# Kernel tuning notes

Hardware: AMD Instinct MI355X
Metric: run time of the kernel (lower is better)

## Reference

```python
import jax, jax.numpy as jnp
import numpy as np

B, L, D, H = 4, 1024, 1024, 16
DK = D // H  # per-head dim = d_q = d_k = d_v = 64


def setup_inputs() -> dict:
    key = jax.random.key(0)
    ks = jax.random.split(key, 11)
    s = 0.02
    return {
        "query": jax.random.normal(ks[0], (B, L, D), jnp.float32),
        "key_in": jax.random.normal(ks[1], (B, L, D), jnp.float32),
        "value": jax.random.normal(ks[2], (B, L, D), jnp.float32),
        # per-head Q/K projection weights stacked: [H, D, DK]
        "wq": jax.random.normal(ks[3], (H, D, DK), jnp.float32) * s,
        "bq": jax.random.normal(ks[4], (H, DK), jnp.float32) * s,
        "wk": jax.random.normal(ks[5], (H, D, DK), jnp.float32) * s,
        "bk": jax.random.normal(ks[6], (H, DK), jnp.float32) * s,
        # shared value projection: [D, DK]
        "wv": jax.random.normal(ks[7], (D, DK), jnp.float32) * s,
        "bv": jax.random.normal(ks[8], (DK,), jnp.float32) * s,
        # output projection: [DK, D]
        "wo": jax.random.normal(ks[9], (DK, D), jnp.float32) * s,
        "bo": jax.random.normal(ks[10], (D,), jnp.float32) * s,
    }


def reference(query, key_in, value, wq, bq, wk, bk, wv, bv, wo, bo):
    dk = wq.shape[-1]
    scale = 1.0 / np.sqrt(dk).astype(np.float32)
    # shared V projection: [B, L, DK]
    v_proj = value @ wv + bv
    # batched per-head Q/K projections (replaces the per-head Linear loop)
    q = jnp.einsum("bld,hdk->bhlk", query, wq) + bq[None, :, None, :]
    k = jnp.einsum("bld,hdk->bhlk", key_in, wk) + bk[None, :, None, :]
    # softmax(QK^T / sqrt(dk)) directly -- equivalent to SDPA with v=eye(L)
    scores = jnp.einsum("bhqk,bhmk->bhqm", q, k) * scale  # [B, H, Lq, Lk]
    attn = jax.nn.softmax(scores, axis=-1)
    # head_i = attn_i @ v_proj : [B, H, Lq, DK]
    heads = jnp.einsum("bhqm,bmv->bhqv", attn, v_proj)
    head_mean = heads.mean(axis=1)  # mean over heads -> [B, Lq, DK]
    output = head_mean @ wo + bo  # [B, Lq, D]
    # match torch stack(dim=2): attn -> [B, Lq, H, Lk]
    attn_out = jnp.transpose(attn, (0, 2, 1, 3))
    return output, attn_out
```

## Files before the change

### kernel.cpp

```cpp
#include <hip/hip_runtime.h>
#include <math.h>

#define NB 4
#define NL 1024
#define ND 1024
#define NH 16
#define NDK 64

typedef __attribute__((ext_vector_type(8))) short short8;
typedef __attribute__((ext_vector_type(4))) float f32x4;

__device__ inline ushort f2bf(float f) {
    uint x = __float_as_uint(f);
    x += 0x7FFFu + ((x >> 16) & 1u);
    return (ushort)(x >> 16);
}
__device__ inline float bf2f(ushort u) { return __uint_as_float(((uint)u) << 16); }

__device__ inline void gload16(const void* g, void* l) {
    __builtin_amdgcn_global_load_lds(
        (const __attribute__((address_space(1))) void*)g,
        (__attribute__((address_space(3))) void*)l, 16, 0, 0);
}

__global__ __launch_bounds__(256) void prep_kernel(
    const float* __restrict__ q, const float* __restrict__ k,
    const float* __restrict__ v,
    const float* __restrict__ wq, const float* __restrict__ wk,
    const float* __restrict__ wv,
    ushort* __restrict__ abf,
    ushort* __restrict__ wqT, ushort* __restrict__ wkT, ushort* __restrict__ wvT)
{
    __shared__ ushort tl[64][72];
    const int t = threadIdx.x;
    const int bid = blockIdx.x;

    if (bid < 6144) {
        int y = bid >> 11, x = bid & 2047;
        const float* src = (y == 0) ? q : (y == 1) ? k : v;
        size_t base = ((size_t)x * 256 + t) * 8;
        float4 a = *(const float4*)(src + base);
        float4 b = *(const float4*)(src + base + 4);
        short8 o;
        o[0] = (short)f2bf(a.x); o[1] = (short)f2bf(a.y);
        o[2] = (short)f2bf(a.z); o[3] = (short)f2bf(a.w);
        o[4] = (short)f2bf(b.x); o[5] = (short)f2bf(b.y);
        o[6] = (short)f2bf(b.z); o[7] = (short)f2bf(b.w);
        *(short8*)(abf + (size_t)y * (NB * NL * ND) + base) = o;
        return;
    }

    int id = bid - 6144;
    int d0 = (id & 15) * 64;
    int y = id >> 4;
    const float* src; ushort* dst; int h;
    if (y < 16)      { src = wq + (size_t)y * ND * NDK;        dst = wqT; h = y; }
    else if (y < 32) { src = wk + (size_t)(y - 16) * ND * NDK; dst = wkT; h = y - 16; }
    else             { src = wv;                               dst = wvT; h = 0; }

    int r = t >> 2, c0 = (t & 3) * 16;
    const float* s = src + (size_t)(d0 + r) * NDK + c0;
    #pragma unroll
    for (int j = 0; j < 16; j += 4) {
        float4 vv4 = *(const float4*)(s + j);
        tl[c0 + j + 0][r] = f2bf(vv4.x);
        tl[c0 + j + 1][r] = f2bf(vv4.y);
        tl[c0 + j + 2][r] = f2bf(vv4.z);
        tl[c0 + j + 3][r] = f2bf(vv4.w);
    }
    __syncthreads();
    int vv = t >> 2, lc = (t & 3) * 16;
    ushort* d = dst + ((size_t)h * 64 + vv) * ND + d0 + lc;
    #pragma unroll
    for (int j = 0; j < 16; j += 8) {
        short8 o;
        #pragma unroll
        for (int e = 0; e < 8; ++e) o[e] = (short)tl[vv][lc + j + e];
        *(short8*)(d + j) = o;
    }
    if (y == 32) {
        ushort* zp = wvT + ((size_t)(64 + (t >> 2))) * ND + d0 + (t & 3) * 16;
        short8 z8 = {0,0,0,0,0,0,0,0};
        *(short8*)(zp) = z8;
        *(short8*)(zp + 8) = z8;
    }
}

__global__ __launch_bounds__(256) void proj_gemm(
    const ushort* __restrict__ abf,
    const ushort* __restrict__ wqT, const ushort* __restrict__ wkT,
    const ushort* __restrict__ wvT,
    const float* __restrict__ bq, const float* __restrict__ bk,
    const float* __restrict__ bv,
    ushort* __restrict__ q_all, ushort* __restrict__ k_all,
    ushort* __restrict__ vT)
{
    __shared__ char lds[49152];

    int id = blockIdx.x;
    int wg = (id & 7) * 136 + (id >> 3);
    int z, mt, nt;
    if (wg < 512)       { z = 0; mt = wg >> 3; nt = wg & 7; }
    else if (wg < 1024) { z = 1; int r2 = wg - 512; mt = r2 >> 3; nt = r2 & 7; }
    else                { z = 2; mt = wg - 1024; nt = 0; }

    const ushort* A; const ushort* Bw; const float* bias; float scale;
    if (z == 0)      { A = abf;                    Bw = wqT; bias = bq; scale = 0.125f; }
    else if (z == 1) { A = abf + NB * NL * ND;     Bw = wkT; bias = bk; scale = 1.0f; }
    else             { A = abf + 2 * NB * NL * ND; Bw = wvT; bias = bv; scale = 1.0f; }
    ushort* C = (z == 0) ? q_all : k_all;

    const int t = threadIdx.x;
    const int w = t >> 6, l = t & 63;
    const int lo16 = l & 15, hi = l >> 4;
    const int wm = w >> 1, wn = w & 1;
    const int m0 = mt * 64, n0 = nt * 128;

    f32x4 acc[2][4];
    #pragma unroll
    for (int mi = 0; mi < 2; ++mi)
        #pragma unroll
        for (int ni = 0; ni < 4; ++ni) acc[mi][ni] = (f32x4){0.f, 0.f, 0.f, 0.f};

    const int lrow = l >> 3;
    const uint lcol = ((uint)(l & 7) * 16u) ^ (((uint)lrow) << 4);

    #pragma unroll
    for (int i = 0; i < 2; ++i) {
        int s = w * 2 + i;
        gload16(A + (size_t)(m0 + s * 8 + lrow) * ND + (lcol >> 1), lds + s * 1024);
    }
    #pragma unroll
    for (int i = 0; i < 4; ++i) {
        int s = w * 4 + i;
        gload16(Bw + (size_t)(n0 + s * 8 + lrow) * ND + (lcol >> 1), lds + 8192 + s * 1024);
    }
    __syncthreads();

    int cur = 0;
    for (int kt = 0; kt < 16; ++kt) {
        if (kt < 15) {
            const int k1 = (kt + 1) * 64;
            const int nb = (cur ^ 1) * 24576;
            #pragma unroll
            for (int i = 0; i < 2; ++i) {
                int s = w * 2 + i;
                gload16(A + (size_t)(m0 + s * 8 + lrow) * ND + k1 + (lcol >> 1), lds + nb + s * 1024);
            }
            #pragma unroll
            for (int i = 0; i < 4; ++i) {
                int s = w * 4 + i;
                gload16(Bw + (size_t)(n0 + s * 8 + lrow) * ND + k1 + (lcol >> 1), lds + nb + 8192 + s * 1024);
            }
        }
        const int cb = cur * 24576;
        #pragma unroll
        for (int ks = 0; ks < 2; ++ks) {
            short8 Af[2], Bf[4];
            #pragma unroll
            for (int mi = 0; mi < 2; ++mi) {
                int row = wm * 32 + mi * 16 + lo16;
                uint off = ((uint)row * 128u + (uint)(ks * 64 + hi * 16)) ^ (((uint)(row & 7)) << 4);
                Af[mi] = *(short8*)(lds + cb + off);
            }
            #pragma unroll
            for (int ni = 0; ni < 4; ++ni) {
                int row = wn * 64 + ni * 16 + lo16;
                uint off = ((uint)row * 128u + (uint)(ks * 64 + hi * 16)) ^ (((uint)(row & 7)) << 4);
                Bf[ni] = *(short8*)(lds + cb + 8192 + off);
            }
            __builtin_amdgcn_s_setprio(1);
            #pragma unroll
            for (int mi = 0; mi < 2; ++mi)
                #pragma unroll
                for (int ni = 0; ni < 4; ++ni)
                    acc[mi][ni] = __builtin_amdgcn_mfma_f32_16x16x32_bf16(
                        Af[mi], Bf[ni], acc[mi][ni], 0, 0, 0);
            __builtin_amdgcn_s_setprio(0);
        }
        __syncthreads();
        cur ^= 1;
    }

    if (z == 2) {
        if (wn == 0) {
            #pragma unroll
            for (int ni = 0; ni < 4; ++ni) {
                int n = ni * 16 + lo16;
                float bs = bias[n];
                #pragma unroll
                for (int mi = 0; mi < 2; ++mi) {
                    int mbase = m0 + wm * 32 + mi * 16 + hi * 4;
                    int b = mbase >> 10, ll = mbase & 1023;
                    uint u0 = (uint)f2bf(acc[mi][ni][0] + bs) | ((uint)f2bf(acc[mi][ni][1] + bs) << 16);
                    uint u1 = (uint)f2bf(acc[mi][ni][2] + bs) | ((uint)f2bf(acc[mi][ni][3] + bs) << 16);
                    *(uint2*)(vT + ((size_t)b * NDK + n) * NL + ll) = make_uint2(u0, u1);
                }
            }
        }
        return;
    }

    ushort* cst = (ushort*)lds;
    const int n0w = wn * 64;
    #pragma unroll
    for (int ni = 0; ni < 4; ++ni) {
        int nl = n0w + ni * 16 + lo16;
        float bs = bias[n0 + nl];
        #pragma unroll
        for (int mi = 0; mi < 2; ++mi) {
            int mlb = wm * 32 + mi * 16 + hi * 4;
            #pragma unroll
            for (int r = 0; r < 4; ++r)
                cst[(mlb + r) * 128 + nl] = f2bf((acc[mi][ni][r] + bs) * scale);
        }
    }
    __syncthreads();
    #pragma unroll
    for (int i = 0; i < 4; ++i) {
        int unit = t + 256 * i;
        int row = unit >> 4, s8 = unit & 15;
        short8 v = *(short8*)(cst + row * 128 + s8 * 8);
        int m = m0 + row, n = n0 + s8 * 8;
        int b = m >> 10, ll = m & 1023, h = n >> 6, dk = n & 63;
        *(short8*)(C + (((size_t)b * NH + h) * NL + ll) * NDK + dk) = v;
    }
}

__global__ __launch_bounds__(256) void attn_mfma_kernel(
    const ushort* __restrict__ q_all, const ushort* __restrict__ k_all,
    const ushort* __restrict__ vT,
    float* __restrict__ attn, ushort* __restrict__ heads)
{
    __shared__ char raw[65536 + 640];
    float* smv  = (float*)(raw + 65536);
    float* invb = (float*)(raw + 65536 + 512);

    const int t = threadIdx.x;
    const int kh = t >> 6, l = t & 63;
    const int hi = l >> 4, lo = l & 15;
    const int h  = blockIdx.x;
    const int q0 = blockIdx.y * 32;
    const int b  = blockIdx.z;
    const size_t bh = ((size_t)b * NH + h) * NL;

    const int qrA = lo;
    const int qrB = 16 + lo;
    const uint swz = ((uint)(lo & 7)) << 4;

    short8 QA0 = *(const short8*)(q_all + (bh + q0 + qrA) * NDK + hi * 8);
    short8 QA1 = *(const short8*)(q_all + (bh + q0 + qrA) * NDK + 32 + hi * 8);
    short8 QB0 = *(const short8*)(q_all + (bh + q0 + qrB) * NDK + hi * 8);
    short8 QB1 = *(const short8*)(q_all + (bh + q0 + qrB) * NDK + 32 + hi * 8);

    float ssumA = 0.f, ssumB = 0.f;
    for (int kt = 0; kt < 16; ++kt) {
        const int kbase = kh * 256 + kt * 16;
        short8 Ka0 = *(const short8*)(k_all + (bh + kbase + lo) * NDK + hi * 8);
        short8 Ka1 = *(const short8*)(k_all + (bh + kbase + lo) * NDK + 32 + hi * 8);
        f32x4 sA = {0.f, 0.f, 0.f, 0.f};
        f32x4 sB = {0.f, 0.f, 0.f, 0.f};
        __builtin_amdgcn_s_setprio(1);
        sA = __builtin_amdgcn_mfma_f32_16x16x32_bf16(Ka0, QA0, sA, 0, 0, 0);
        sA = __builtin_amdgcn_mfma_f32_16x16x32_bf16(Ka1, QA1, sA, 0, 0, 0);
        sB = __builtin_amdgcn_mfma_f32_16x16x32_bf16(Ka0, QB0, sB, 0, 0, 0);
        sB = __builtin_amdgcn_mfma_f32_16x16x32_bf16(Ka1, QB1, sB, 0, 0, 0);
        __builtin_amdgcn_s_setprio(0);
        float a0 = __expf(sA[0]), a1 = __expf(sA[1]);
        float a2 = __expf(sA[2]), a3 = __expf(sA[3]);
        float b0 = __expf(sB[0]), b1 = __expf(sB[1]);
        float b2 = __expf(sB[2]), b3 = __expf(sB[3]);
        ssumA += (a0 + a1) + (a2 + a3);
        ssumB += (b0 + b1) + (b2 + b3);
        uint colb = (((uint)(kbase + hi * 4)) * 2u) ^ swz;
        *(uint2*)(raw + (uint)qrA * 2048u + colb) =
            make_uint2((uint)f2bf(a0) | ((uint)f2bf(a1) << 16),
                       (uint)f2bf(a2) | ((uint)f2bf(a3) << 16));
        *(uint2*)(raw + (uint)qrB * 2048u + colb) =
            make_uint2((uint)f2bf(b0) | ((uint)f2bf(b1) << 16),
                       (uint)f2bf(b2) | ((uint)f2bf(b3) << 16));
    }
    ssumA += __shfl_xor(ssumA, 16);
    ssumA += __shfl_xor(ssumA, 32);
    ssumB += __shfl_xor(ssumB, 16);
    ssumB += __shfl_xor(ssumB, 32);
    if (l < 16) {
        smv[kh * 32 + l]      = ssumA;
        smv[kh * 32 + 16 + l] = ssumB;
    }
    __syncthreads();
    if (t < 32) invb[t] = 1.0f / (smv[t] + smv[32 + t] + smv[64 + t] + smv[96 + t]);
    __syncthreads();

    f32x4 accA0 = {0.f,0.f,0.f,0.f}, accA1 = {0.f,0.f,0.f,0.f};
    f32x4 accA2 = {0.f,0.f,0.f,0.f}, accA3 = {0.f,0.f,0.f,0.f};
    f32x4 accB0 = {0.f,0.f,0.f,0.f}, accB1 = {0.f,0.f,0.f,0.f};
    f32x4 accB2 = {0.f,0.f,0.f,0.f}, accB3 = {0.f,0.f,0.f,0.f};
    for (int kc = 0; kc < 8; ++kc) {
        const int kchunk = kh * 256 + kc * 32;
        uint colb = (((uint)(kchunk + hi * 8)) * 2u) ^ swz;
        short8 paA = *(short8*)(raw + (uint)qrA * 2048u + colb);
        short8 paB = *(short8*)(raw + (uint)qrB * 2048u + colb);
        short8 b0 = *(const short8*)(vT + ((size_t)(b * NDK +  0 + lo)) * NL + kchunk + hi * 8);
        short8 b1 = *(const short8*)(vT + ((size_t)(b * NDK + 16 + lo)) * NL + kchunk + hi * 8);
        short8 b2 = *(const short8*)(vT + ((size_t)(b * NDK + 32 + lo)) * NL + kchunk + hi * 8);
        short8 b3 = *(const short8*)(vT + ((size_t)(b * NDK + 48 + lo)) * NL + kchunk + hi * 8);
        __builtin_amdgcn_s_setprio(1);
        accA0 = __builtin_amdgcn_mfma_f32_16x16x32_bf16(paA, b0, accA0, 0, 0, 0);
        accA1 = __builtin_amdgcn_mfma_f32_16x16x32_bf16(paA, b1, accA1, 0, 0, 0);
        accA2 = __builtin_amdgcn_mfma_f32_16x16x32_bf16(paA, b2, accA2, 0, 0, 0);
        accA3 = __builtin_amdgcn_mfma_f32_16x16x32_bf16(paA, b3, accA3, 0, 0, 0);
        accB0 = __builtin_amdgcn_mfma_f32_16x16x32_bf16(paB, b0, accB0, 0, 0, 0);
        accB1 = __builtin_amdgcn_mfma_f32_16x16x32_bf16(paB, b1, accB1, 0, 0, 0);
        accB2 = __builtin_amdgcn_mfma_f32_16x16x32_bf16(paB, b2, accB2, 0, 0, 0);
        accB3 = __builtin_amdgcn_mfma_f32_16x16x32_bf16(paB, b3, accB3, 0, 0, 0);
        __builtin_amdgcn_s_setprio(0);
        #pragma unroll
        for (int rj = 0; rj < 4; ++rj) {
            int rr = kc * 4 + rj;
            uint byteoff = (uint)rr * 2048u + (((uint)t * 8u) ^ (((uint)(rr & 7)) << 4));
            uint2 v = *(uint2*)(raw + byteoff);
            float inv = invb[rr];
            f32x4 o;
            o[0] = bf2f((ushort)(v.x & 0xFFFF)) * inv;
            o[1] = bf2f((ushort)(v.x >> 16)) * inv;
            o[2] = bf2f((ushort)(v.y & 0xFFFF)) * inv;
            o[3] = bf2f((ushort)(v.y >> 16)) * inv;
            __builtin_nontemporal_store(o,
                (f32x4*)(attn + (((size_t)b * NL + q0 + rr) * NH + h) * NL + (size_t)t * 4));
        }
    }
    __syncthreads();
    float* pvp = (float*)raw;
    #pragma unroll
    for (int r = 0; r < 4; ++r) {
        int rowA = kh * 32 + hi * 4 + r;
        pvp[rowA * 68 +  0 + lo] = accA0[r];
        pvp[rowA * 68 + 16 + lo] = accA1[r];
        pvp[rowA * 68 + 32 + lo] = accA2[r];
        pvp[rowA * 68 + 48 + lo] = accA3[r];
        int rowB = rowA + 16;
        pvp[rowB * 68 +  0 + lo] = accB0[r];
        pvp[rowB * 68 + 16 + lo] = accB1[r];
        pvp[rowB * 68 + 32 + lo] = accB2[r];
        pvp[rowB * 68 + 48 + lo] = accB3[r];
    }
    __syncthreads();
    #pragma unroll
    for (int i = 0; i < 8; ++i) {
        int idx = t + 256 * i;
        int qq = idx >> 6, vv = idx & 63;
        float s4 = pvp[qq * 68 + vv] + pvp[(32 + qq) * 68 + vv]
                 + pvp[(64 + qq) * 68 + vv] + pvp[(96 + qq) * 68 + vv];
        heads[(bh + q0 + qq) * NDK + vv] = f2bf(s4 * invb[qq]);
    }
}

__global__ __launch_bounds__(256) void out_proj_kernel(
    const ushort* __restrict__ heads, const float* __restrict__ wo,
    const float* __restrict__ bo, float* __restrict__ out)
{
    const int t = threadIdx.x;
    const int row0 = blockIdx.x * 8;
    const int b = row0 >> 10, l0 = row0 & 1023;
    __shared__ float hm[8][64];
    if (t < 128) {
        int r = t >> 4;
        int f4 = t & 15;
        float sx = 0.f, sy = 0.f, sz = 0.f, sw = 0.f;
        #pragma unroll
        for (int h = 0; h < 16; ++h) {
            uint2 v = *(const uint2*)&heads[(((size_t)b * NH + h) * NL + l0 + r) * NDK + f4 * 4];
            sx += bf2f((ushort)(v.x & 0xFFFF));
            sy += bf2f((ushort)(v.x >> 16));
            sz += bf2f((ushort)(v.y & 0xFFFF));
            sw += bf2f((ushort)(v.y >> 16));
        }
        float4 o; o.x = sx * 0.0625f; o.y = sy * 0.0625f; o.z = sz * 0.0625f; o.w = sw * 0.0625f;
        *(float4*)&hm[r][f4 * 4] = o;
    }
    __syncthreads();

    float acc[8][4];
    #pragma unroll
    for (int r = 0; r < 8; ++r)
        #pragma unroll
        for (int j = 0; j < 4; ++j) acc[r][j] = 0.f;

    for (int k = 0; k < 64; ++k) {
        float w0 = wo[(size_t)k * ND + t];
        float w1 = wo[(size_t)k * ND + t + 256];
        float w2 = wo[(size_t)k * ND + t + 512];
        float w3 = wo[(size_t)k * ND + t + 768];
        #pragma unroll
        for (int r = 0; r < 8; ++r) {
            float hv = hm[r][k];
            acc[r][0] += hv * w0;
            acc[r][1] += hv * w1;
            acc[r][2] += hv * w2;
            acc[r][3] += hv * w3;
        }
    }
    #pragma unroll
    for (int r = 0; r < 8; ++r) {
        out[((size_t)row0 + r) * ND + t      ] = acc[r][0] + bo[t];
        out[((size_t)row0 + r) * ND + t + 256] = acc[r][1] + bo[t + 256];
        out[((size_t)row0 + r) * ND + t + 512] = acc[r][2] + bo[t + 512];
        out[((size_t)row0 + r) * ND + t + 768] = acc[r][3] + bo[t + 768];
    }
}

extern "C" void kernel_launch(void* const* d_in, const int* in_sizes, int n_in,
                              void* d_out, int out_size, void* d_ws, size_t ws_size,
                              hipStream_t stream) {
    const float* query  = (const float*)d_in[0];
    const float* key_in = (const float*)d_in[1];
    const float* value  = (const float*)d_in[2];
    const float* wq     = (const float*)d_in[3];
    const float* bq     = (const float*)d_in[4];
    const float* wk     = (const float*)d_in[5];
    const float* bk     = (const float*)d_in[6];
    const float* wv     = (const float*)d_in[7];
    const float* bv     = (const float*)d_in[8];
    const float* wo     = (const float*)d_in[9];
    const float* bo     = (const float*)d_in[10];

    float* out  = (float*)d_out;
    float* attn = out + (size_t)NB * NL * ND;

    ushort* wqT    = (ushort*)d_ws;
    ushort* wkT    = wqT + (size_t)ND * NH * NDK;
    ushort* wvT    = wkT + (size_t)ND * NH * NDK;
    ushort* q_all  = wvT + (size_t)128 * ND;
    ushort* k_all  = q_all + (size_t)NB * NH * NL * NDK;
    ushort* vT     = k_all + (size_t)NB * NH * NL * NDK;
    ushort* abf    = vT + (size_t)NB * NDK * NL;
    ushort* heads  = abf;

    prep_kernel<<<dim3(6672), 256, 0, stream>>>(
        query, key_in, value, wq, wk, wv, abf, wqT, wkT, wvT);
    proj_gemm<<<dim3(1088), 256, 0, stream>>>(
        abf, wqT, wkT, wvT, bq, bk, bv, q_all, k_all, vT);
    attn_mfma_kernel<<<dim3(NH, NL / 32, NB), 256, 0, stream>>>(
        q_all, k_all, vT, attn, heads);
    out_proj_kernel<<<dim3(NB * NL / 8), 256, 0, stream>>>(
        heads, wo, bo, out);
}
```

Before: 138.6 us.

## Fuse fp32-to-bf16 activation conversion into projection GEMM A-tile loads

Drops the separate pass that converted query/key/value to bf16 in a workspace buffer. The projection GEMM now reads fp32 activations directly into registers for the next K-tile, converts them to bf16 after the current tile's MFMAs, and writes them into the swizzled LDS buffer. This removes a full write and re-read of the bf16 activation copy and shrinks the prep launch to weights only. In exchange, the GEMM reads twice the bytes per A tile through registers instead of async global-to-LDS loads, and does extra conversion work inside the main loop. Each A tile is also re-read by the eight N-tiles of its row.

Result: slower. 148.3 us (+7.0%).

```diff
diff --git a/kernel.cpp b/kernel.cpp
--- a/kernel.cpp
+++ b/kernel.cpp
@@ -24,33 +24,13 @@
 }
 
 __global__ __launch_bounds__(256) void prep_kernel(
-    const float* __restrict__ q, const float* __restrict__ k,
-    const float* __restrict__ v,
     const float* __restrict__ wq, const float* __restrict__ wk,
     const float* __restrict__ wv,
-    ushort* __restrict__ abf,
     ushort* __restrict__ wqT, ushort* __restrict__ wkT, ushort* __restrict__ wvT)
 {
     __shared__ ushort tl[64][72];
     const int t = threadIdx.x;
-    const int bid = blockIdx.x;
-
-    if (bid < 6144) {
-        int y = bid >> 11, x = bid & 2047;
-        const float* src = (y == 0) ? q : (y == 1) ? k : v;
-        size_t base = ((size_t)x * 256 + t) * 8;
-        float4 a = *(const float4*)(src + base);
-        float4 b = *(const float4*)(src + base + 4);
-        short8 o;
-        o[0] = (short)f2bf(a.x); o[1] = (short)f2bf(a.y);
-        o[2] = (short)f2bf(a.z); o[3] = (short)f2bf(a.w);
-        o[4] = (short)f2bf(b.x); o[5] = (short)f2bf(b.y);
-        o[6] = (short)f2bf(b.z); o[7] = (short)f2bf(b.w);
-        *(short8*)(abf + (size_t)y * (NB * NL * ND) + base) = o;
-        return;
-    }
-
-    int id = bid - 6144;
+    int id = blockIdx.x;
     int d0 = (id & 15) * 64;
     int y = id >> 4;
     const float* src; ushort* dst; int h;
@@ -87,7 +67,8 @@
 }
 
 __global__ __launch_bounds__(256) void proj_gemm(
-    const ushort* __restrict__ abf,
+    const float* __restrict__ query, const float* __restrict__ key_in,
+    const float* __restrict__ value,
     const ushort* __restrict__ wqT, const ushort* __restrict__ wkT,
     const ushort* __restrict__ wvT,
     const float* __restrict__ bq, const float* __restrict__ bk,
@@ -104,10 +85,10 @@
     else if (wg < 1024) { z = 1; int r2 = wg - 512; mt = r2 >> 3; nt = r2 & 7; }
     else                { z = 2; mt = wg - 1024; nt = 0; }
 
-    const ushort* A; const ushort* Bw; const float* bias; float scale;
-    if (z == 0)      { A = abf;                    Bw = wqT; bias = bq; scale = 0.125f; }
-    else if (z == 1) { A = abf + NB * NL * ND;     Bw = wkT; bias = bk; scale = 1.0f; }
-    else             { A = abf + 2 * NB * NL * ND; Bw = wvT; bias = bv; scale = 1.0f; }
+    const float* A; const ushort* Bw; const float* bias; float scale;
+    if (z == 0)      { A = query;  Bw = wqT; bias = bq; scale = 0.125f; }
+    else if (z == 1) { A = key_in; Bw = wkT; bias = bk; scale = 1.0f; }
+    else             { A = value;  Bw = wvT; bias = bv; scale = 1.0f; }
     ushort* C = (z == 0) ? q_all : k_all;
 
     const int t = threadIdx.x;
@@ -125,28 +106,43 @@
     const int lrow = l >> 3;
     const uint lcol = ((uint)(l & 7) * 16u) ^ (((uint)lrow) << 4);
 
-    #pragma unroll
-    for (int i = 0; i < 2; ++i) {
-        int s = w * 2 + i;
-        gload16(A + (size_t)(m0 + s * 8 + lrow) * ND + (lcol >> 1), lds + s * 1024);
-    }
-    #pragma unroll
-    for (int i = 0; i < 4; ++i) {
-        int s = w * 4 + i;
-        gload16(Bw + (size_t)(n0 + s * 8 + lrow) * ND + (lcol >> 1), lds + 8192 + s * 1024);
+    const int ar0 = (2 * t) >> 3, ac0 = (2 * t) & 7;
+    const int ar1 = (2 * t + 1) >> 3, ac1 = (2 * t + 1) & 7;
+    const uint aoff0 = ((uint)ar0 * 128u + (uint)ac0 * 16u) ^ (((uint)(ar0 & 7)) << 4);
+    const uint aoff1 = ((uint)ar1 * 128u + (uint)ac1 * 16u) ^ (((uint)(ar1 & 7)) << 4);
+    const float* arow0 = A + (size_t)(m0 + ar0) * ND + ac0 * 8;
+    const float* arow1 = A + (size_t)(m0 + ar1) * ND + ac1 * 8;
+
+    {
+        float4 a00 = *(const float4*)(arow0);
+        float4 a01 = *(const float4*)(arow0 + 4);
+        float4 a10 = *(const float4*)(arow1);
+        float4 a11 = *(const float4*)(arow1 + 4);
+        short8 o0, o1;
+        o0[0]=(short)f2bf(a00.x); o0[1]=(short)f2bf(a00.y); o0[2]=(short)f2bf(a00.z); o0[3]=(short)f2bf(a00.w);
+        o0[4]=(short)f2bf(a01.x); o0[5]=(short)f2bf(a01.y); o0[6]=(short)f2bf(a01.z); o0[7]=(short)f2bf(a01.w);
+        o1[0]=(short)f2bf(a10.x); o1[1]=(short)f2bf(a10.y); o1[2]=(short)f2bf(a10.z); o1[3]=(short)f2bf(a10.w);
+        o1[4]=(short)f2bf(a11.x); o1[5]=(short)f2bf(a11.y); o1[6]=(short)f2bf(a11.z); o1[7]=(short)f2bf(a11.w);
+        *(short8*)(lds + aoff0) = o0;
+        *(short8*)(lds + aoff1) = o1;
+        #pragma unroll
+        for (int i = 0; i < 4; ++i) {
+            int s = w * 4 + i;
+            gload16(Bw + (size_t)(n0 + s * 8 + lrow) * ND + (lcol >> 1), lds + 8192 + s * 1024);
+        }
     }
     __syncthreads();
 
     int cur = 0;
     for (int kt = 0; kt < 16; ++kt) {
+        float4 a00, a01, a10, a11;
+        const int nb = (cur ^ 1) * 24576;
         if (kt < 15) {
             const int k1 = (kt + 1) * 64;
-            const int nb = (cur ^ 1) * 24576;
-            #pragma unroll
-            for (int i = 0; i < 2; ++i) {
-                int s = w * 2 + i;
-                gload16(A + (size_t)(m0 + s * 8 + lrow) * ND + k1 + (lcol >> 1), lds + nb + s * 1024);
-            }
+            a00 = *(const float4*)(arow0 + k1);
+            a01 = *(const float4*)(arow0 + k1 + 4);
+            a10 = *(const float4*)(arow1 + k1);
+            a11 = *(const float4*)(arow1 + k1 + 4);
             #pragma unroll
             for (int i = 0; i < 4; ++i) {
                 int s = w * 4 + i;
@@ -177,6 +173,15 @@
                     acc[mi][ni] = __builtin_amdgcn_mfma_f32_16x16x32_bf16(
                         Af[mi], Bf[ni], acc[mi][ni], 0, 0, 0);
             __builtin_amdgcn_s_setprio(0);
+        }
+        if (kt < 15) {
+            short8 o0, o1;
+            o0[0]=(short)f2bf(a00.x); o0[1]=(short)f2bf(a00.y); o0[2]=(short)f2bf(a00.z); o0[3]=(short)f2bf(a00.w);
+            o0[4]=(short)f2bf(a01.x); o0[5]=(short)f2bf(a01.y); o0[6]=(short)f2bf(a01.z); o0[7]=(short)f2bf(a01.w);
+            o1[0]=(short)f2bf(a10.x); o1[1]=(short)f2bf(a10.y); o1[2]=(short)f2bf(a10.z); o1[3]=(short)f2bf(a10.w);
+            o1[4]=(short)f2bf(a11.x); o1[5]=(short)f2bf(a11.y); o1[6]=(short)f2bf(a11.z); o1[7]=(short)f2bf(a11.w);
+            *(short8*)(lds + nb + aoff0) = o0;
+            *(short8*)(lds + nb + aoff1) = o1;
         }
         __syncthreads();
         cur ^= 1;
@@ -434,13 +439,11 @@
     ushort* q_all  = wvT + (size_t)128 * ND;
     ushort* k_all  = q_all + (size_t)NB * NH * NL * NDK;
     ushort* vT     = k_all + (size_t)NB * NH * NL * NDK;
-    ushort* abf    = vT + (size_t)NB * NDK * NL;
-    ushort* heads  = abf;
-
-    prep_kernel<<<dim3(6672), 256, 0, stream>>>(
-        query, key_in, value, wq, wk, wv, abf, wqT, wkT, wvT);
+    ushort* heads  = vT + (size_t)NB * NDK * NL;
+
+    prep_kernel<<<dim3(528), 256, 0, stream>>>(wq, wk, wv, wqT, wkT, wvT);
     proj_gemm<<<dim3(1088), 256, 0, stream>>>(
-        abf, wqT, wkT, wvT, bq, bk, bv, q_all, k_all, vT);
+        query, key_in, value, wqT, wkT, wvT, bq, bk, bv, q_all, k_all, vT);
     attn_mfma_kernel<<<dim3(NH, NL / 32, NB), 256, 0, stream>>>(
         q_all, k_all, vT, attn, heads);
     out_proj_kernel<<<dim3(NB * NL / 8), 256, 0, stream>>>(
```

## Use bf16 MFMA for output projection with pre-transposed bf16 Wo

Applied to the files above, without the earlier changes.

The prep kernel gains 16 extra blocks that convert Wo to bf16 and transpose it to an [N][K] layout. The output projection now stages the bf16 head mean in swizzled LDS and computes each 32x256 tile with 16x16x32 bf16 MFMA instructions, replacing the scalar FP32 FMA loop over 8-row tiles. This moves the output GEMM onto matrix cores and cuts Wo read traffic. The cost is extra rounding of the head mean and Wo to bf16, plus more prep work.

Measured after the change: 136.5 us (median of 2 runs). Within noise of the previous version (-1.5%).

```diff
diff --git a/kernel.cpp b/kernel.cpp
--- a/kernel.cpp
+++ b/kernel.cpp
@@ -27,9 +27,10 @@
     const float* __restrict__ q, const float* __restrict__ k,
     const float* __restrict__ v,
     const float* __restrict__ wq, const float* __restrict__ wk,
-    const float* __restrict__ wv,
+    const float* __restrict__ wv, const float* __restrict__ wo,
     ushort* __restrict__ abf,
-    ushort* __restrict__ wqT, ushort* __restrict__ wkT, ushort* __restrict__ wvT)
+    ushort* __restrict__ wqT, ushort* __restrict__ wkT,
+    ushort* __restrict__ wvT, ushort* __restrict__ woT)
 {
     __shared__ ushort tl[64][72];
     const int t = threadIdx.x;
@@ -53,6 +54,31 @@
     int id = bid - 6144;
     int d0 = (id & 15) * 64;
     int y = id >> 4;
+
+    if (y == 33) {
+        int kr = t >> 2, c0 = (t & 3) * 16;
+        const float* s = wo + (size_t)kr * ND + d0 + c0;
+        #pragma unroll
+        for (int j = 0; j < 16; j += 4) {
+            float4 vv4 = *(const float4*)(s + j);
+            tl[c0 + j + 0][kr] = f2bf(vv4.x);
+            tl[c0 + j + 1][kr] = f2bf(vv4.y);
+            tl[c0 + j + 2][kr] = f2bf(vv4.z);
+            tl[c0 + j + 3][kr] = f2bf(vv4.w);
+        }
+        __syncthreads();
+        int vv = t >> 2, lc = (t & 3) * 16;
+        ushort* d = woT + (size_t)(d0 + vv) * NDK + lc;
+        #pragma unroll
+        for (int j = 0; j < 16; j += 8) {
+            short8 o;
+            #pragma unroll
+            for (int e = 0; e < 8; ++e) o[e] = (short)tl[vv][lc + j + e];
+            *(short8*)(d + j) = o;
+        }
+        return;
+    }
+
     const float* src; ushort* dst; int h;
     if (y < 16)      { src = wq + (size_t)y * ND * NDK;        dst = wqT; h = y; }
     else if (y < 32) { src = wk + (size_t)(y - 16) * ND * NDK; dst = wkT; h = y - 16; }
@@ -357,56 +383,66 @@
 }
 
 __global__ __launch_bounds__(256) void out_proj_kernel(
-    const ushort* __restrict__ heads, const float* __restrict__ wo,
+    const ushort* __restrict__ heads, const ushort* __restrict__ woT,
     const float* __restrict__ bo, float* __restrict__ out)
 {
+    __shared__ char lds[4096];
     const int t = threadIdx.x;
-    const int row0 = blockIdx.x * 8;
-    const int b = row0 >> 10, l0 = row0 & 1023;
-    __shared__ float hm[8][64];
-    if (t < 128) {
-        int r = t >> 4;
-        int f4 = t & 15;
-        float sx = 0.f, sy = 0.f, sz = 0.f, sw = 0.f;
+    const int w = t >> 6, l = t & 63;
+    const int lo16 = l & 15, hi = l >> 4;
+    const int rt = blockIdx.x >> 2, ct = blockIdx.x & 3;
+    const int m0 = rt * 32, n0 = ct * 256;
+    const int b = m0 >> 10, l0 = m0 & 1023;
+
+    {
+        int r = t >> 3, qd = t & 7;
+        float s[8] = {0.f,0.f,0.f,0.f,0.f,0.f,0.f,0.f};
         #pragma unroll
         for (int h = 0; h < 16; ++h) {
-            uint2 v = *(const uint2*)&heads[(((size_t)b * NH + h) * NL + l0 + r) * NDK + f4 * 4];
-            sx += bf2f((ushort)(v.x & 0xFFFF));
-            sy += bf2f((ushort)(v.x >> 16));
-            sz += bf2f((ushort)(v.y & 0xFFFF));
-            sw += bf2f((ushort)(v.y >> 16));
-        }
-        float4 o; o.x = sx * 0.0625f; o.y = sy * 0.0625f; o.z = sz * 0.0625f; o.w = sw * 0.0625f;
-        *(float4*)&hm[r][f4 * 4] = o;
-    }
-    __syncthreads();
-
-    float acc[8][4];
-    #pragma unroll
-    for (int r = 0; r < 8; ++r)
-        #pragma unroll
-        for (int j = 0; j < 4; ++j) acc[r][j] = 0.f;
-
-    for (int k = 0; k < 64; ++k) {
-        float w0 = wo[(size_t)k * ND + t];
-        float w1 = wo[(size_t)k * ND + t + 256];
-        float w2 = wo[(size_t)k * ND + t + 512];
-        float w3 = wo[(size_t)k * ND + t + 768];
-        #pragma unroll
-        for (int r = 0; r < 8; ++r) {
-            float hv = hm[r][k];
-            acc[r][0] += hv * w0;
-            acc[r][1] += hv * w1;
-            acc[r][2] += hv * w2;
-            acc[r][3] += hv * w3;
-        }
-    }
-    #pragma unroll
-    for (int r = 0; r < 8; ++r) {
-        out[((size_t)row0 + r) * ND + t      ] = acc[r][0] + bo[t];
-        out[((size_t)row0 + r) * ND + t + 256] = acc[r][1] + bo[t + 256];
-        out[((size_t)row0 + r) * ND + t + 512] = acc[r][2] + bo[t + 512];
-        out[((size_t)row0 + r) * ND + t + 768] = acc[r][3] + bo[t + 768];
+            uint4 v = *(const uint4*)&heads[(((size_t)b * NH + h) * NL + l0 + r) * NDK + qd * 8];
+            s[0] += bf2f((ushort)(v.x & 0xFFFF)); s[1] += bf2f((ushort)(v.x >> 16));
+            s[2] += bf2f((ushort)(v.y & 0xFFFF)); s[3] += bf2f((ushort)(v.y >> 16));
+            s[4] += bf2f((ushort)(v.z & 0xFFFF)); s[5] += bf2f((ushort)(v.z >> 16));
+            s[6] += bf2f((ushort)(v.w & 0xFFFF)); s[7] += bf2f((ushort)(v.w >> 16));
+        }
+        short8 o;
+        #pragma unroll
+        for (int e = 0; e < 8; ++e) o[e] = (short)f2bf(s[e] * 0.0625f);
+        uint off = ((uint)r * 128u + (uint)qd * 16u) ^ (((uint)(r & 7)) << 4);
+        *(short8*)(lds + off) = o;
+    }
+    __syncthreads();
+
+    const int wr = (w & 1) * 16, wc = (w >> 1) * 128;
+    short8 Af[2];
+    {
+        int row = wr + lo16;
+        #pragma unroll
+        for (int ks = 0; ks < 2; ++ks) {
+            uint off = ((uint)row * 128u + (uint)(ks * 64 + hi * 16)) ^ (((uint)(row & 7)) << 4);
+            Af[ks] = *(short8*)(lds + off);
+        }
+    }
+    f32x4 acc[8];
+    #pragma unroll
+    for (int ni = 0; ni < 8; ++ni) acc[ni] = (f32x4){0.f, 0.f, 0.f, 0.f};
+    #pragma unroll
+    for (int ni = 0; ni < 8; ++ni) {
+        int n = n0 + wc + ni * 16 + lo16;
+        short8 B0 = *(const short8*)(woT + (size_t)n * NDK + hi * 8);
+        short8 B1 = *(const short8*)(woT + (size_t)n * NDK + 32 + hi * 8);
+        acc[ni] = __builtin_amdgcn_mfma_f32_16x16x32_bf16(Af[0], B0, acc[ni], 0, 0, 0);
+        acc[ni] = __builtin_amdgcn_mfma_f32_16x16x32_bf16(Af[1], B1, acc[ni], 0, 0, 0);
+    }
+    #pragma unroll
+    for (int ni = 0; ni < 8; ++ni) {
+        int n = n0 + wc + ni * 16 + lo16;
+        float bs = bo[n];
+        #pragma unroll
+        for (int r = 0; r < 4; ++r) {
+            int m = m0 + wr + hi * 4 + r;
+            out[(size_t)m * ND + n] = acc[ni][r] + bs;
+        }
     }
 }
 
@@ -431,18 +467,19 @@
     ushort* wqT    = (ushort*)d_ws;
     ushort* wkT    = wqT + (size_t)ND * NH * NDK;
     ushort* wvT    = wkT + (size_t)ND * NH * NDK;
-    ushort* q_all  = wvT + (size_t)128 * ND;
+    ushort* woT    = wvT + (size_t)128 * ND;
+    ushort* q_all  = woT + (size_t)ND * NDK;
     ushort* k_all  = q_all + (size_t)NB * NH * NL * NDK;
     ushort* vT     = k_all + (size_t)NB * NH * NL * NDK;
     ushort* abf    = vT + (size_t)NB * NDK * NL;
     ushort* heads  = abf;
 
-    prep_kernel<<<dim3(6672), 256, 0, stream>>>(
-        query, key_in, value, wq, wk, wv, abf, wqT, wkT, wvT);
+    prep_kernel<<<dim3(6688), 256, 0, stream>>>(
+        query, key_in, value, wq, wk, wv, wo, abf, wqT, wkT, wvT, woT);
     proj_gemm<<<dim3(1088), 256, 0, stream>>>(
         abf, wqT, wkT, wvT, bq, bk, bv, q_all, k_all, vT);
     attn_mfma_kernel<<<dim3(NH, NL / 32, NB), 256, 0, stream>>>(
         q_all, k_all, vT, attn, heads);
-    out_proj_kernel<<<dim3(NB * NL / 8), 256, 0, stream>>>(
-        heads, wo, bo, out);
-}
+    out_proj_kernel<<<dim3(512), 256, 0, stream>>>(
+        heads, woT, bo, out);
+}
```
